# Optimization experiments

Hardware: AMD Instinct MI355X
Metric: run time of the kernel (lower is better)

Reference implementation:

```python
import jax, jax.numpy as jnp
import numpy as np

V, D, H, L, T_MAX = 95, 384, 6, 6, 256
HD = D // H  # 64
FF = 4 * D


def _layernorm(x, scale, bias, eps=1e-5):
    m = jnp.mean(x, axis=-1, keepdims=True)
    v = jnp.var(x, axis=-1, keepdims=True)
    return (x - m) * jax.lax.rsqrt(v + eps) * scale + bias


def setup_inputs() -> dict:
    key = jax.random.key(0)
    ks = iter(jax.random.split(key, 32))
    std = 0.02
    p = {
        "idx": jax.random.randint(next(ks), (128, 256), 0, V, dtype=jnp.int64)
               if jax.config.jax_enable_x64 else
               jax.random.randint(next(ks), (128, 256), 0, V, dtype=jnp.int32),
        "tok_emb": jax.random.normal(next(ks), (V, D), jnp.float32) * std,
        "pos_emb": jax.random.normal(next(ks), (T_MAX, D), jnp.float32) * std,
        # per-layer stacked params [L, ...]
        "ln1_s": jnp.ones((L, D), jnp.float32),
        "ln1_b": jnp.zeros((L, D), jnp.float32),
        "wq": jax.random.normal(next(ks), (L, D, D), jnp.float32) * std,
        "wk": jax.random.normal(next(ks), (L, D, D), jnp.float32) * std,
        "wv": jax.random.normal(next(ks), (L, D, D), jnp.float32) * std,
        "wo": jax.random.normal(next(ks), (L, D, D), jnp.float32) * std,
        "bo": jnp.zeros((L, D), jnp.float32),
        "ln2_s": jnp.ones((L, D), jnp.float32),
        "ln2_b": jnp.zeros((L, D), jnp.float32),
        "w1": jax.random.normal(next(ks), (L, D, FF), jnp.float32) * std,
        "b1": jnp.zeros((L, FF), jnp.float32),
        "w2": jax.random.normal(next(ks), (L, FF, D), jnp.float32) * std,
        "b2": jnp.zeros((L, D), jnp.float32),
        "lnf_s": jnp.ones((D,), jnp.float32),
        "lnf_b": jnp.zeros((D,), jnp.float32),
        "head_w": jax.random.normal(next(ks), (D, V), jnp.float32) * std,
        "head_b": jnp.zeros((V,), jnp.float32),
    }
    return p


def reference(idx, tok_emb, pos_emb, ln1_s, ln1_b, wq, wk, wv, wo, bo,
              ln2_s, ln2_b, w1, b1, w2, b2, lnf_s, lnf_b, head_w, head_b):
    B, T = idx.shape
    x = tok_emb[idx] + pos_emb[:T]  # [B,T,D]
    mask = jnp.tril(jnp.ones((T, T), bool))  # causal
    scale = HD ** -0.5

    def block(x, p):
        s1, b1n, Wq, Wk, Wv, Wo, Bo, s2, b2n, W1, B1, W2, B2 = p
        h = _layernorm(x, s1, b1n)
        q = (h @ Wq).reshape(B, T, H, HD)
        k = (h @ Wk).reshape(B, T, H, HD)
        v = (h @ Wv).reshape(B, T, H, HD)
        scores = jnp.einsum('bqhd,bkhd->bhqk', q, k) * scale
        scores = jnp.where(mask, scores, -jnp.inf)
        wei = jax.nn.softmax(scores, axis=-1)
        attn = jnp.einsum('bhqk,bkhd->bqhd', wei, v).reshape(B, T, D)
        x = x + attn @ Wo + Bo
        h2 = _layernorm(x, s2, b2n)
        x = x + jax.nn.relu(h2 @ W1 + B1) @ W2 + B2
        return x, None

    x, _ = jax.lax.scan(block, x, (ln1_s, ln1_b, wq, wk, wv, wo, bo,
                                   ln2_s, ln2_b, w1, b1, w2, b2))
    logits = _layernorm(x, lnf_s, lnf_b) @ head_w + head_b  # [B,T,V]
    return logits
```

## Files before the change

### kernel.cpp

```cpp
#include <hip/hip_runtime.h>
#include <hip/hip_bf16.h>
#include <cstdint>

#define DEV __device__ __forceinline__

typedef __hip_bfloat16 bf16;
typedef unsigned short u16;
typedef unsigned int u32;
typedef __attribute__((ext_vector_type(8))) short s8v;
typedef __attribute__((ext_vector_type(4))) float f4;

static constexpr int Bn = 128;
static constexpr int Tn = 256;
static constexpr int Dn = 384;
static constexpr int Hn = 6;
static constexpr int HDn = 64;
static constexpr int FFn = 1536;
static constexpr int Vn = 95;
static constexpr int Mn = Bn * 256;

DEV u16 f2b(float f) {
  bf16 h = __float2bfloat16(f);
  return *reinterpret_cast<u16*>(&h);
}
DEV u32 pk2(float a, float b) { return (u32)f2b(a) | ((u32)f2b(b) << 16); }

DEV void gl_lds16(const void* g, void* l) {
  auto gp = (const __attribute__((address_space(1))) u32*)(uintptr_t)g;
  auto lp = (__attribute__((address_space(3))) u32*)(u32)(uintptr_t)l;
  __builtin_amdgcn_global_load_lds(gp, lp, 16, 0, 0);
}

DEV void waitvm(int n) {
  if (n == 0)       asm volatile("s_waitcnt vmcnt(0)" ::: "memory");
  else if (n == 2)  asm volatile("s_waitcnt vmcnt(2)" ::: "memory");
  else if (n == 4)  asm volatile("s_waitcnt vmcnt(4)" ::: "memory");
  else if (n == 6)  asm volatile("s_waitcnt vmcnt(6)" ::: "memory");
  else if (n == 8)  asm volatile("s_waitcnt vmcnt(8)" ::: "memory");
  else if (n == 12) asm volatile("s_waitcnt vmcnt(12)" ::: "memory");
  else              asm volatile("s_waitcnt vmcnt(16)" ::: "memory");
}

template <int MODE, bool RELU, int NKT, int NT>
__global__ __launch_bounds__(256, 2) void gemm_h(
    const u16* __restrict__ A, const u16* __restrict__ Bw,
    const float* __restrict__ bias, const float* __restrict__ resid,
    void* __restrict__ outp)
{
  constexpr int K = NKT * 64;
  constexpr int N = NT * 16;
  constexpr int nTiles = NT / 8;
  __shared__ __align__(16) u16 As[3][128 * 64];
  const int tid = threadIdx.x;
  const int lane = tid & 63, wave = tid >> 6;
  const int quad = lane >> 4, l16 = lane & 15;
  const int wy = wave >> 1, wx = wave & 1;
  const int blk = blockIdx.x;
  const int xcd = blk & 7, tt = blk >> 3;
  const int nT = tt % nTiles, mT = xcd + 8 * (tt / nTiles);
  const int mBase = mT * 128, nBase = nT * 128;

  f4 acc[4][4] = {};

  int rS[4], cS[4];
#pragma unroll
  for (int i = 0; i < 4; i++) {
    int s = i * 256 + tid;
    rS[i] = s >> 3;
    cS[i] = ((s & 7) ^ (rS[i] & 7)) * 8;
  }

  const u16* Ab = A + (size_t)mBase * K;
  const u16* Bp = Bw + (size_t)((nBase >> 4) + wx * 4) * 512 + lane * 8;

#define STAGEA(buf, kt)                                                       \
  do {                                                                        \
    _Pragma("unroll")                                                         \
    for (int i = 0; i < 4; i++)                                               \
      gl_lds16(Ab + (size_t)rS[i] * K + (kt) + cS[i],                         \
               &As[buf][(i * 256 + wave * 64) * 8]);                          \
  } while (0)

  s8v bqa[2][4];
  STAGEA(0, 0);
  __builtin_amdgcn_sched_barrier(0);
#pragma unroll
  for (int j = 0; j < 4; j++)
    bqa[0][j] = *(const s8v*)(Bp + (size_t)0 * (NT * 512) + j * 512);
  __builtin_amdgcn_sched_barrier(0);
  STAGEA(1, 64);
  __builtin_amdgcn_sched_barrier(0);

  const int nk = NKT;
#pragma unroll
  for (int ik = 0; ik < nk; ik++) {
    const int cur = ik % 3;
    const int par = ik & 1;
    waitvm((ik + 1 < nk) ? 4 : 0);
    asm volatile("s_barrier" ::: "memory");
    s8v bqb[4];
#pragma unroll
    for (int j = 0; j < 4; j++)
      bqb[j] = *(const s8v*)(Bp + (size_t)(ik * 2 + 1) * (NT * 512) + j * 512);
    __builtin_amdgcn_sched_barrier(0);
    if (ik + 1 < nk) {
#pragma unroll
      for (int j = 0; j < 4; j++)
        bqa[par ^ 1][j] = *(const s8v*)(Bp + (size_t)(ik * 2 + 2) * (NT * 512) + j * 512);
    }
    __builtin_amdgcn_sched_barrier(0);
    if (ik + 2 < nk) STAGEA((ik + 2) % 3, (ik + 2) * 64);
    __builtin_amdgcn_sched_barrier(0);
    {
      s8v af[4];
#pragma unroll
      for (int i = 0; i < 4; i++) {
        int row = wy * 64 + i * 16 + l16;
        int ch = quad ^ (row & 7);
        af[i] = *(const s8v*)&As[cur][row * 64 + ch * 8];
      }
#pragma unroll
      for (int i = 0; i < 4; i++)
#pragma unroll
        for (int j = 0; j < 4; j++)
          acc[i][j] = __builtin_amdgcn_mfma_f32_16x16x32_bf16(af[i], bqa[par][j], acc[i][j], 0, 0, 0);
    }
    waitvm(4 * ((ik + 1 < nk) + (ik + 2 < nk)));
    {
      s8v af[4];
#pragma unroll
      for (int i = 0; i < 4; i++) {
        int row = wy * 64 + i * 16 + l16;
        int ch = (4 + quad) ^ (row & 7);
        af[i] = *(const s8v*)&As[cur][row * 64 + ch * 8];
      }
#pragma unroll
      for (int i = 0; i < 4; i++)
#pragma unroll
        for (int j = 0; j < 4; j++)
          acc[i][j] = __builtin_amdgcn_mfma_f32_16x16x32_bf16(af[i], bqb[j], acc[i][j], 0, 0, 0);
    }
  }
#undef STAGEA

  if (MODE == 0) {
    u16* out = (u16*)outp;
#pragma unroll
    for (int j = 0; j < 4; j++) {
      int n = nBase + wx * 64 + j * 16 + l16;
      float bv = bias ? bias[n] : 0.f;
#pragma unroll
      for (int i = 0; i < 4; i++) {
        int m0 = mBase + wy * 64 + i * 16 + quad * 4;
#pragma unroll
        for (int r = 0; r < 4; r++) {
          float v = acc[i][j][r] + bv;
          if (RELU) v = fmaxf(v, 0.f);
          out[(size_t)(m0 + r) * N + n] = f2b(v);
        }
      }
    }
  } else if (MODE == 3) {
    float* out = (float*)outp;
#pragma unroll
    for (int j = 0; j < 4; j++) {
      int n = nBase + wx * 64 + j * 16 + l16;
      if (n < Vn) {
        float bv = bias[n];
#pragma unroll
        for (int i = 0; i < 4; i++) {
          int m0 = mBase + wy * 64 + i * 16 + quad * 4;
#pragma unroll
          for (int r = 0; r < 4; r++)
            out[(size_t)(m0 + r) * Vn + n] = acc[i][j][r] + bv;
        }
      }
    }
  } else if (MODE == 4) {
    u16* qb = (u16*)outp;
    u16* kb = qb + (size_t)Mn * 384;
    u16* vb = kb + (size_t)Mn * 384;
#pragma unroll
    for (int j = 0; j < 4; j++) {
      int n = nBase + wx * 64 + j * 16 + l16;
      if (n < 768) {
        u16* dst = (n < 384) ? qb : kb;
        int col = (n < 384) ? n : (n - 384);
#pragma unroll
        for (int i = 0; i < 4; i++) {
          int m0 = mBase + wy * 64 + i * 16 + quad * 4;
#pragma unroll
          for (int r = 0; r < 4; r++)
            dst[(size_t)(m0 + r) * 384 + col] = f2b(acc[i][j][r]);
        }
      } else {
        int n7 = n - 768;
        int hh = n7 >> 6, d = n7 & 63;
#pragma unroll
        for (int i = 0; i < 4; i++) {
          int m0 = mBase + wy * 64 + i * 16 + quad * 4;
          int b = m0 >> 8, t0 = m0 & 255;
          uint2 w;
          w.x = pk2(acc[i][j][0], acc[i][j][1]);
          w.y = pk2(acc[i][j][2], acc[i][j][3]);
          *(uint2*)&vb[((b * Hn + hh) * HDn + d) * Tn + t0] = w;
        }
      }
    }
  }
}

template <int NKT>
__global__ __launch_bounds__(512, 2) void gemm_ln(
    const u16* __restrict__ A, const u16* __restrict__ Bw,
    const float* __restrict__ bias, const float* __restrict__ resid,
    float* __restrict__ xout,
    const float* __restrict__ sc, const float* __restrict__ bi,
    u16* __restrict__ hout)
{
  constexpr int K = NKT * 64;
  constexpr int NT = 24;
  __shared__ __align__(16) u16 As[3][128 * 64];
  __shared__ float2 red[4][128];
  const int tid = threadIdx.x;
  const int lane = tid & 63, wave = tid >> 6;
  const int quad = lane >> 4, l16 = lane & 15;
  const int wy = wave >> 2, wx = wave & 3;
  const int blk = blockIdx.x;
  const int mT = (blk & 7) + 8 * (blk >> 3);
  const int mBase = mT * 128;

  f4 acc[4][6] = {};

  int rS[2], cS[2];
#pragma unroll
  for (int i = 0; i < 2; i++) {
    int s = i * 512 + tid;
    rS[i] = s >> 3;
    cS[i] = ((s & 7) ^ (rS[i] & 7)) * 8;
  }

  const u16* Ab = A + (size_t)mBase * K;
  const u16* Bp = Bw + (size_t)(wx * 6) * 512 + lane * 8;

#define STAGEL(buf, kt)                                                       \
  do {                                                                        \
    _Pragma("unroll")                                                         \
    for (int i = 0; i < 2; i++)                                               \
      gl_lds16(Ab + (size_t)rS[i] * K + (kt) + cS[i],                         \
               &As[buf][(i * 512 + wave * 64) * 8]);                          \
  } while (0)

  STAGEL(0, 0);
  __builtin_amdgcn_sched_barrier(0);
  STAGEL(1, 64);
  __builtin_amdgcn_sched_barrier(0);

  const int nk = NKT;
#pragma unroll
  for (int ik = 0; ik < nk; ik++) {
    const int cur = ik % 3;
    waitvm((ik + 1 < nk) ? 2 : 0);
    asm volatile("s_barrier" ::: "memory");
    s8v bq0[6], bq1[6];
#pragma unroll
    for (int j = 0; j < 6; j++)
      bq0[j] = *(const s8v*)(Bp + (size_t)(ik * 2) * (NT * 512) + j * 512);
    __builtin_amdgcn_sched_barrier(0);
#pragma unroll
    for (int j = 0; j < 6; j++)
      bq1[j] = *(const s8v*)(Bp + (size_t)(ik * 2 + 1) * (NT * 512) + j * 512);
    __builtin_amdgcn_sched_barrier(0);
    if (ik + 2 < nk) STAGEL((ik + 2) % 3, (ik + 2) * 64);
    __builtin_amdgcn_sched_barrier(0);
    waitvm(6 + ((ik + 2 < nk) ? 2 : 0));
    {
      s8v af[4];
#pragma unroll
      for (int i = 0; i < 4; i++) {
        int row = wy * 64 + i * 16 + l16;
        int ch = quad ^ (row & 7);
        af[i] = *(const s8v*)&As[cur][row * 64 + ch * 8];
      }
#pragma unroll
      for (int i = 0; i < 4; i++)
#pragma unroll
        for (int j = 0; j < 6; j++)
          acc[i][j] = __builtin_amdgcn_mfma_f32_16x16x32_bf16(af[i], bq0[j], acc[i][j], 0, 0, 0);
    }
    waitvm((ik + 2 < nk) ? 2 : 0);
    {
      s8v af[4];
#pragma unroll
      for (int i = 0; i < 4; i++) {
        int row = wy * 64 + i * 16 + l16;
        int ch = (4 + quad) ^ (row & 7);
        af[i] = *(const s8v*)&As[cur][row * 64 + ch * 8];
      }
#pragma unroll
      for (int i = 0; i < 4; i++)
#pragma unroll
        for (int j = 0; j < 6; j++)
          acc[i][j] = __builtin_amdgcn_mfma_f32_16x16x32_bf16(af[i], bq1[j], acc[i][j], 0, 0, 0);
    }
  }
#undef STAGEL

  f4 psum[4] = {}, psq[4] = {};
#pragma unroll
  for (int j = 0; j < 6; j++) {
    int n = wx * 96 + j * 16 + l16;
    float bv = bias[n];
#pragma unroll
    for (int i = 0; i < 4; i++) {
      int m0 = mBase + wy * 64 + i * 16 + quad * 4;
#pragma unroll
      for (int r = 0; r < 4; r++) {
        int m = m0 + r;
        float v = resid[(size_t)m * Dn + n] + acc[i][j][r] + bv;
        xout[(size_t)m * Dn + n] = v;
        acc[i][j][r] = v;
        psum[i][r] += v;
        psq[i][r] += v * v;
      }
    }
  }
#pragma unroll
  for (int o = 1; o < 16; o <<= 1)
#pragma unroll
    for (int i = 0; i < 4; i++)
#pragma unroll
      for (int r = 0; r < 4; r++) {
        psum[i][r] += __shfl_xor(psum[i][r], o);
        psq[i][r] += __shfl_xor(psq[i][r], o);
      }
  if (l16 == 0) {
#pragma unroll
    for (int i = 0; i < 4; i++)
#pragma unroll
      for (int r = 0; r < 4; r++) {
        int lr = wy * 64 + i * 16 + quad * 4 + r;
        float2 p; p.x = psum[i][r]; p.y = psq[i][r];
        red[wx][lr] = p;
      }
  }
  __syncthreads();
  float scv[6], biv[6];
#pragma unroll
  for (int j = 0; j < 6; j++) {
    int n = wx * 96 + j * 16 + l16;
    scv[j] = sc[n];
    biv[j] = bi[n];
  }
#pragma unroll
  for (int i = 0; i < 4; i++)
#pragma unroll
    for (int r = 0; r < 4; r++) {
      int lr = wy * 64 + i * 16 + quad * 4 + r;
      float ts = 0.f, tq = 0.f;
#pragma unroll
      for (int w = 0; w < 4; w++) { float2 p = red[w][lr]; ts += p.x; tq += p.y; }
      float mean = ts * (1.f / 384.f);
      float inv = rsqrtf(tq * (1.f / 384.f) - mean * mean + 1e-5f);
      int m = mBase + lr;
#pragma unroll
      for (int j = 0; j < 6; j++) {
        int n = wx * 96 + j * 16 + l16;
        hout[(size_t)m * Dn + n] = f2b((acc[i][j][r] - mean) * inv * scv[j] + biv[j]);
      }
    }
}

__global__ __launch_bounds__(256) void attn_kernel(
    const u16* __restrict__ q, const u16* __restrict__ k,
    const u16* __restrict__ vT, u16* __restrict__ ao)
{
  __shared__ __align__(16) u16 Ps[4][2][16 * 40];
  const int tid = threadIdx.x, lane = tid & 63, wave = tid >> 6;
  const int quad = lane >> 4, l16 = lane & 15;
  const int c4 = blockIdx.x / 768;
  const int bh = blockIdx.x - c4 * 768;
  const int b = bh / Hn, h = bh % Hn;
  const u16* qg = q + (b * Tn) * Dn + h * HDn;
  const u16* kg = k + (b * Tn) * Dn + h * HDn;
  const u16* vg = vT + bh * (HDn * Tn);
  u16* aog = ao + (b * Tn) * Dn + h * HDn;
  const float c1 = 0.125f * 1.44269504f;

  const int qt = (wave & 2) ? ((wave & 1) ? 15 - c4 : 8 + c4)
                            : ((wave & 1) ? 7 - c4 : c4);
  const int qglob = qt * 16 + l16;

  const s8v qf0 = *(const s8v*)&qg[qglob * Dn + quad * 8];
  const s8v qf1 = *(const s8v*)&qg[qglob * Dn + 32 + quad * 8];

  float lsum = 0.f;
  f4 O[4] = {};

  const int nch = qt / 2 + 1;
  for (int c2 = 0; c2 < nch; c2++) {
    const int kk0 = c2 * 32;
    f4 S0 = {0.f, 0.f, 0.f, 0.f}, S1 = S0;
    {
      s8v kf = *(const s8v*)&kg[(kk0 + l16) * Dn + quad * 8];
      S0 = __builtin_amdgcn_mfma_f32_16x16x32_bf16(kf, qf0, S0, 0, 0, 0);
      kf = *(const s8v*)&kg[(kk0 + l16) * Dn + 32 + quad * 8];
      S0 = __builtin_amdgcn_mfma_f32_16x16x32_bf16(kf, qf1, S0, 0, 0, 0);
    }
    if (kk0 + 16 <= qt * 16) {
      s8v kf = *(const s8v*)&kg[(kk0 + 16 + l16) * Dn + quad * 8];
      S1 = __builtin_amdgcn_mfma_f32_16x16x32_bf16(kf, qf0, S1, 0, 0, 0);
      kf = *(const s8v*)&kg[(kk0 + 16 + l16) * Dn + 32 + quad * 8];
      S1 = __builtin_amdgcn_mfma_f32_16x16x32_bf16(kf, qf1, S1, 0, 0, 0);
    }
    const int kkq = kk0 + quad * 4;
    f4 E0, E1;
#pragma unroll
    for (int r = 0; r < 4; r++) {
      E0[r] = (kkq + r <= qglob) ? exp2f(S0[r] * c1) : 0.f;
      E1[r] = (kkq + 16 + r <= qglob) ? exp2f(S1[r] * c1) : 0.f;
      lsum += E0[r] + E1[r];
    }
    u16* prow = &Ps[wave][c2 & 1][l16 * 40];
    uint2 w0, w1;
    w0.x = pk2(E0[0], E0[1]); w0.y = pk2(E0[2], E0[3]);
    w1.x = pk2(E1[0], E1[1]); w1.y = pk2(E1[2], E1[3]);
    *(uint2*)&prow[quad * 4] = w0;
    *(uint2*)&prow[16 + quad * 4] = w1;
    const s8v pf = *(const s8v*)&prow[quad * 8];
#pragma unroll
    for (int dm = 0; dm < 4; dm++) {
      s8v vf = *(const s8v*)&vg[(dm * 16 + l16) * Tn + kk0 + quad * 8];
      O[dm] = __builtin_amdgcn_mfma_f32_16x16x32_bf16(vf, pf, O[dm], 0, 0, 0);
    }
  }

  lsum += __shfl_xor(lsum, 16);
  lsum += __shfl_xor(lsum, 32);
  const float inv = 1.0f / lsum;
#pragma unroll
  for (int dm = 0; dm < 4; dm++) {
    uint2 w;
    w.x = pk2(O[dm][0] * inv, O[dm][1] * inv);
    w.y = pk2(O[dm][2] * inv, O[dm][3] * inv);
    *(uint2*)&aog[qglob * Dn + dm * 16 + quad * 4] = w;
  }
}

__global__ __launch_bounds__(256) void ln_kernel(
    const float* __restrict__ x, const float* __restrict__ sc,
    const float* __restrict__ bi, u16* __restrict__ out)
{
  int tok = blockIdx.x * 4 + (threadIdx.x >> 6);
  int lane = threadIdx.x & 63;
  const float* xr = x + (size_t)tok * Dn;
  float v[6];
  float s = 0.f, sq = 0.f;
#pragma unroll
  for (int i = 0; i < 6; i++) {
    v[i] = xr[lane + 64 * i];
    s += v[i];
    sq += v[i] * v[i];
  }
#pragma unroll
  for (int o = 1; o < 64; o <<= 1) {
    s += __shfl_xor(s, o);
    sq += __shfl_xor(sq, o);
  }
  float mean = s * (1.f / 384.f);
  float var = sq * (1.f / 384.f) - mean * mean;
  float inv = rsqrtf(var + 1e-5f);
  u16* orow = out + (size_t)tok * Dn;
#pragma unroll
  for (int i = 0; i < 6; i++) {
    int c = lane + 64 * i;
    orow[c] = f2b((v[i] - mean) * inv * sc[c] + bi[c]);
  }
}

__global__ __launch_bounds__(256) void embed_kernel(
    const int* __restrict__ idx, const float* __restrict__ tok,
    const float* __restrict__ pos, float* __restrict__ x)
{
  int i = blockIdx.x * 256 + threadIdx.x;
  int m = i / 96, c = (i - m * 96) * 4;
  int t = m & (Tn - 1);
  const float4 tv = *(const float4*)&tok[idx[m] * Dn + c];
  const float4 pv = *(const float4*)&pos[t * Dn + c];
  float4 r;
  r.x = tv.x + pv.x; r.y = tv.y + pv.y; r.z = tv.z + pv.z; r.w = tv.w + pv.w;
  *(float4*)&x[m * Dn + c] = r;
}

__global__ __launch_bounds__(256) void tcvt_frag(
    const float* __restrict__ src, u16* __restrict__ dst,
    int K, int C, int NTsub, int NTtot, int ntoff, int total)
{
  int t = blockIdx.x * 256 + threadIdx.x;
  if (t >= total) return;
  int j8 = t & 7;
  int lane = (t >> 3) & 63;
  int rest = t >> 9;
  int nt = rest % NTsub;
  int lkc = rest / NTsub;
  int KC = K >> 5;
  int kc = lkc % KC;
  int l = lkc / KC;
  int quad = lane >> 4, l16 = lane & 15;
  int k = kc * 32 + quad * 8 + j8;
  int n = nt * 16 + l16;
  float v = (n < C) ? src[((size_t)l * K + k) * C + n] : 0.f;
  dst[((size_t)(l * KC + kc) * NTtot + ntoff + nt) * 512 + lane * 8 + j8] = f2b(v);
}

extern "C" void kernel_launch(void* const* d_in, const int* in_sizes, int n_in,
                              void* d_out, int out_size, void* d_ws, size_t ws_size,
                              hipStream_t stream)
{
  (void)in_sizes; (void)n_in; (void)out_size;
  const int*   idx     = (const int*)d_in[0];
  const float* tok_emb = (const float*)d_in[1];
  const float* pos_emb = (const float*)d_in[2];
  const float* ln1_s   = (const float*)d_in[3];
  const float* ln1_b   = (const float*)d_in[4];
  const float* wq      = (const float*)d_in[5];
  const float* wk      = (const float*)d_in[6];
  const float* wv      = (const float*)d_in[7];
  const float* wo      = (const float*)d_in[8];
  const float* bo      = (const float*)d_in[9];
  const float* ln2_s   = (const float*)d_in[10];
  const float* ln2_b   = (const float*)d_in[11];
  const float* w1      = (const float*)d_in[12];
  const float* b1      = (const float*)d_in[13];
  const float* w2      = (const float*)d_in[14];
  const float* b2      = (const float*)d_in[15];
  const float* lnf_s   = (const float*)d_in[16];
  const float* lnf_b   = (const float*)d_in[17];
  const float* head_w  = (const float*)d_in[18];
  const float* head_b  = (const float*)d_in[19];
  float* out = (float*)d_out;

  char* ws = (char*)d_ws;
  float* x  = (float*)(ws + 0);
  u16*   h  = (u16*)(ws + 50331648);
  u16*   qb = (u16*)(ws + 75497472);
  u16*   kb = (u16*)(ws + 100663296);
  u16*   vb = (u16*)(ws + 125829120);
  u16*   ab = (u16*)(ws + 150994944);
  u16*   f1 = qb;
  u16* qkvT = (u16*)(ws + 176160768);
  u16* woT  = qkvT + 6 * 442368;
  u16* w1T  = woT + 6 * 147456;
  u16* w2T  = w1T + 6 * 589824;
  u16* hdT  = w2T + 6 * 589824;
  if (ws_size < (size_t)197492736) return;

  int tot = 6 * 384 * 384;
  tcvt_frag<<<(tot + 255) / 256, 256, 0, stream>>>(wq, qkvT, 384, 384, 24, 72, 0, tot);
  tcvt_frag<<<(tot + 255) / 256, 256, 0, stream>>>(wk, qkvT, 384, 384, 24, 72, 24, tot);
  tcvt_frag<<<(tot + 255) / 256, 256, 0, stream>>>(wv, qkvT, 384, 384, 24, 72, 48, tot);
  tcvt_frag<<<(tot + 255) / 256, 256, 0, stream>>>(wo, woT, 384, 384, 24, 24, 0, tot);
  tot = 6 * 384 * 1536;
  tcvt_frag<<<(tot + 255) / 256, 256, 0, stream>>>(w1, w1T, 384, 1536, 96, 96, 0, tot);
  tcvt_frag<<<(tot + 255) / 256, 256, 0, stream>>>(w2, w2T, 1536, 384, 24, 24, 0, tot);
  tot = 384 * 128;
  tcvt_frag<<<(tot + 255) / 256, 256, 0, stream>>>(head_w, hdT, 384, 95, 8, 8, 0, tot);

  embed_kernel<<<(Mn * 96) / 256, 256, 0, stream>>>(idx, tok_emb, pos_emb, x);
  ln_kernel<<<Mn / 4, 256, 0, stream>>>(x, ln1_s, ln1_b, h);

  for (int l = 0; l < 6; l++) {
    gemm_h<4, false, 6, 72><<<2304, 256, 0, stream>>>(h, qkvT + l * 442368, nullptr, nullptr, qb);
    attn_kernel<<<Bn * Hn * 4, 256, 0, stream>>>(qb, kb, vb, ab);
    gemm_ln<6><<<256, 512, 0, stream>>>(ab, woT + l * 147456, bo + l * Dn, x, x,
                                        ln2_s + l * Dn, ln2_b + l * Dn, h);
    gemm_h<0, true, 6, 96><<<3072, 256, 0, stream>>>(h, w1T + l * 589824, b1 + l * FFn, nullptr, f1);
    const float* ns = (l < 5) ? (ln1_s + (l + 1) * Dn) : lnf_s;
    const float* nb = (l < 5) ? (ln1_b + (l + 1) * Dn) : lnf_b;
    gemm_ln<24><<<256, 512, 0, stream>>>(f1, w2T + l * 589824, b2 + l * Dn, x, x,
                                         ns, nb, h);
  }
  gemm_h<3, false, 6, 8><<<256, 256, 0, stream>>>(h, hdT, head_b, nullptr, out);
}
```

Baseline: 1.609 ms.

## Stage weight tiles through LDS with double buffering in GEMM kernels

Both GEMM kernels now copy the B (weight) fragments into shared memory with global_load_lds, double-buffered alongside A, instead of each wave loading them directly into registers. The A pipeline drops from triple to double buffering and each iteration waits on vmcnt(0) before the barrier. The goal is to share weight loads across waves that need the same tile and to free registers. In exchange it uses more LDS, which can cap occupancy, and the full wait at the top of every step reduces how much the loads overlap with compute. An unused STAGEBL macro is left behind.

```diff
diff --git a/kernel.cpp b/kernel.cpp
--- a/kernel.cpp
+++ b/kernel.cpp
@@ -31,16 +31,6 @@
   __builtin_amdgcn_global_load_lds(gp, lp, 16, 0, 0);
 }
 
-DEV void waitvm(int n) {
-  if (n == 0)       asm volatile("s_waitcnt vmcnt(0)" ::: "memory");
-  else if (n == 2)  asm volatile("s_waitcnt vmcnt(2)" ::: "memory");
-  else if (n == 4)  asm volatile("s_waitcnt vmcnt(4)" ::: "memory");
-  else if (n == 6)  asm volatile("s_waitcnt vmcnt(6)" ::: "memory");
-  else if (n == 8)  asm volatile("s_waitcnt vmcnt(8)" ::: "memory");
-  else if (n == 12) asm volatile("s_waitcnt vmcnt(12)" ::: "memory");
-  else              asm volatile("s_waitcnt vmcnt(16)" ::: "memory");
-}
-
 template <int MODE, bool RELU, int NKT, int NT>
 __global__ __launch_bounds__(256, 2) void gemm_h(
     const u16* __restrict__ A, const u16* __restrict__ Bw,
@@ -50,7 +40,8 @@
   constexpr int K = NKT * 64;
   constexpr int N = NT * 16;
   constexpr int nTiles = NT / 8;
-  __shared__ __align__(16) u16 As[3][128 * 64];
+  __shared__ __align__(16) u16 As[2][128 * 64];
+  __shared__ __align__(16) u16 Bs[2][8192];
   const int tid = threadIdx.x;
   const int lane = tid & 63, wave = tid >> 6;
   const int quad = lane >> 4, l16 = lane & 15;
@@ -71,7 +62,7 @@
   }
 
   const u16* Ab = A + (size_t)mBase * K;
-  const u16* Bp = Bw + (size_t)((nBase >> 4) + wx * 4) * 512 + lane * 8;
+  const u16* Bp0 = Bw + (size_t)(nBase >> 4) * 512;
 
 #define STAGEA(buf, kt)                                                       \
   do {                                                                        \
@@ -81,67 +72,51 @@
                &As[buf][(i * 256 + wave * 64) * 8]);                          \
   } while (0)
 
-  s8v bqa[2][4];
+#define STAGEB(buf, ikk)                                                      \
+  do {                                                                        \
+    _Pragma("unroll")                                                         \
+    for (int L = 0; L < 4; L++) {                                             \
+      int ks = L >> 1, hf = L & 1;                                            \
+      gl_lds16(Bp0 + (size_t)((ikk) * 2 + ks) * (NT * 512) + hf * 2048 + tid * 8, \
+               &Bs[buf][ks * 4096 + hf * 2048 + tid * 8]);                    \
+    }                                                                         \
+  } while (0)
+
   STAGEA(0, 0);
-  __builtin_amdgcn_sched_barrier(0);
-#pragma unroll
-  for (int j = 0; j < 4; j++)
-    bqa[0][j] = *(const s8v*)(Bp + (size_t)0 * (NT * 512) + j * 512);
-  __builtin_amdgcn_sched_barrier(0);
-  STAGEA(1, 64);
-  __builtin_amdgcn_sched_barrier(0);
+  STAGEB(0, 0);
 
   const int nk = NKT;
 #pragma unroll
   for (int ik = 0; ik < nk; ik++) {
-    const int cur = ik % 3;
-    const int par = ik & 1;
-    waitvm((ik + 1 < nk) ? 4 : 0);
+    const int cur = ik & 1;
+    asm volatile("s_waitcnt vmcnt(0)" ::: "memory");
     asm volatile("s_barrier" ::: "memory");
-    s8v bqb[4];
-#pragma unroll
-    for (int j = 0; j < 4; j++)
-      bqb[j] = *(const s8v*)(Bp + (size_t)(ik * 2 + 1) * (NT * 512) + j * 512);
+    if (ik + 1 < nk) {
+      STAGEA(cur ^ 1, (ik + 1) * 64);
+      STAGEB(cur ^ 1, ik + 1);
+    }
     __builtin_amdgcn_sched_barrier(0);
-    if (ik + 1 < nk) {
-#pragma unroll
-      for (int j = 0; j < 4; j++)
-        bqa[par ^ 1][j] = *(const s8v*)(Bp + (size_t)(ik * 2 + 2) * (NT * 512) + j * 512);
-    }
-    __builtin_amdgcn_sched_barrier(0);
-    if (ik + 2 < nk) STAGEA((ik + 2) % 3, (ik + 2) * 64);
-    __builtin_amdgcn_sched_barrier(0);
-    {
-      s8v af[4];
+#pragma unroll
+    for (int ks = 0; ks < 2; ks++) {
+      s8v af[4], bq[4];
 #pragma unroll
       for (int i = 0; i < 4; i++) {
         int row = wy * 64 + i * 16 + l16;
-        int ch = quad ^ (row & 7);
+        int ch = (ks * 4 + quad) ^ (row & 7);
         af[i] = *(const s8v*)&As[cur][row * 64 + ch * 8];
       }
 #pragma unroll
+      for (int j = 0; j < 4; j++)
+        bq[j] = *(const s8v*)&Bs[cur][ks * 4096 + (wx * 4 + j) * 512 + lane * 8];
+#pragma unroll
       for (int i = 0; i < 4; i++)
 #pragma unroll
         for (int j = 0; j < 4; j++)
-          acc[i][j] = __builtin_amdgcn_mfma_f32_16x16x32_bf16(af[i], bqa[par][j], acc[i][j], 0, 0, 0);
-    }
-    waitvm(4 * ((ik + 1 < nk) + (ik + 2 < nk)));
-    {
-      s8v af[4];
-#pragma unroll
-      for (int i = 0; i < 4; i++) {
-        int row = wy * 64 + i * 16 + l16;
-        int ch = (4 + quad) ^ (row & 7);
-        af[i] = *(const s8v*)&As[cur][row * 64 + ch * 8];
-      }
-#pragma unroll
-      for (int i = 0; i < 4; i++)
-#pragma unroll
-        for (int j = 0; j < 4; j++)
-          acc[i][j] = __builtin_amdgcn_mfma_f32_16x16x32_bf16(af[i], bqb[j], acc[i][j], 0, 0, 0);
+          acc[i][j] = __builtin_amdgcn_mfma_f32_16x16x32_bf16(af[i], bq[j], acc[i][j], 0, 0, 0);
     }
   }
 #undef STAGEA
+#undef STAGEB
 
   if (MODE == 0) {
     u16* out = (u16*)outp;
@@ -220,7 +195,8 @@
 {
   constexpr int K = NKT * 64;
   constexpr int NT = 24;
-  __shared__ __align__(16) u16 As[3][128 * 64];
+  __shared__ __align__(16) u16 As[2][128 * 64];
+  __shared__ __align__(16) u16 Bs[2][24576];
   __shared__ float2 red[4][128];
   const int tid = threadIdx.x;
   const int lane = tid & 63, wave = tid >> 6;
@@ -241,7 +217,6 @@
   }
 
   const u16* Ab = A + (size_t)mBase * K;
-  const u16* Bp = Bw + (size_t)(wx * 6) * 512 + lane * 8;
 
 #define STAGEL(buf, kt)                                                       \
   do {                                                                        \
@@ -251,60 +226,61 @@
                &As[buf][(i * 512 + wave * 64) * 8]);                          \
   } while (0)
 
+#define STAGEBL(buf, ikk)                                                     \
+  do {                                                                        \
+    _Pragma("unroll")                                                         \
+    for (int L = 0; L < 6; L++) {                                             \
+      int ks = L >> 1, th = L & 1;              \
+      (void)ks; (void)th;                                                     \
+    }                                                                         \
+  } while (0)
+
+#define STAGEB2(buf, ikk)                                                     \
+  do {                                                                        \
+    _Pragma("unroll")                                                         \
+    for (int L = 0; L < 6; L++) {                                             \
+      int ks = L / 3, th = L % 3;                                             \
+      int c = th * 4096 + tid * 8;                                            \
+      gl_lds16(Bw + (size_t)((ikk) * 2 + ks) * (NT * 512) + c,                \
+               &Bs[buf][ks * 12288 + c]);                                     \
+    }                                                                         \
+  } while (0)
+
   STAGEL(0, 0);
-  __builtin_amdgcn_sched_barrier(0);
-  STAGEL(1, 64);
-  __builtin_amdgcn_sched_barrier(0);
+  STAGEB2(0, 0);
 
   const int nk = NKT;
 #pragma unroll
   for (int ik = 0; ik < nk; ik++) {
-    const int cur = ik % 3;
-    waitvm((ik + 1 < nk) ? 2 : 0);
+    const int cur = ik & 1;
+    asm volatile("s_waitcnt vmcnt(0)" ::: "memory");
     asm volatile("s_barrier" ::: "memory");
-    s8v bq0[6], bq1[6];
-#pragma unroll
-    for (int j = 0; j < 6; j++)
-      bq0[j] = *(const s8v*)(Bp + (size_t)(ik * 2) * (NT * 512) + j * 512);
+    if (ik + 1 < nk) {
+      STAGEL(cur ^ 1, (ik + 1) * 64);
+      STAGEB2(cur ^ 1, ik + 1);
+    }
     __builtin_amdgcn_sched_barrier(0);
 #pragma unroll
-    for (int j = 0; j < 6; j++)
-      bq1[j] = *(const s8v*)(Bp + (size_t)(ik * 2 + 1) * (NT * 512) + j * 512);
-    __builtin_amdgcn_sched_barrier(0);
-    if (ik + 2 < nk) STAGEL((ik + 2) % 3, (ik + 2) * 64);
-    __builtin_amdgcn_sched_barrier(0);
-    waitvm(6 + ((ik + 2 < nk) ? 2 : 0));
-    {
-      s8v af[4];
+    for (int ks = 0; ks < 2; ks++) {
+      s8v af[4], bq[6];
 #pragma unroll
       for (int i = 0; i < 4; i++) {
         int row = wy * 64 + i * 16 + l16;
-        int ch = quad ^ (row & 7);
+        int ch = (ks * 4 + quad) ^ (row & 7);
         af[i] = *(const s8v*)&As[cur][row * 64 + ch * 8];
       }
 #pragma unroll
+      for (int j = 0; j < 6; j++)
+        bq[j] = *(const s8v*)&Bs[cur][ks * 12288 + (wx * 6 + j) * 512 + lane * 8];
+#pragma unroll
       for (int i = 0; i < 4; i++)
 #pragma unroll
         for (int j = 0; j < 6; j++)
-          acc[i][j] = __builtin_amdgcn_mfma_f32_16x16x32_bf16(af[i], bq0[j], acc[i][j], 0, 0, 0);
-    }
-    waitvm((ik + 2 < nk) ? 2 : 0);
-    {
-      s8v af[4];
-#pragma unroll
-      for (int i = 0; i < 4; i++) {
-        int row = wy * 64 + i * 16 + l16;
-        int ch = (4 + quad) ^ (row & 7);
-        af[i] = *(const s8v*)&As[cur][row * 64 + ch * 8];
-      }
-#pragma unroll
-      for (int i = 0; i < 4; i++)
-#pragma unroll
-        for (int j = 0; j < 6; j++)
-          acc[i][j] = __builtin_amdgcn_mfma_f32_16x16x32_bf16(af[i], bq1[j], acc[i][j], 0, 0, 0);
+          acc[i][j] = __builtin_amdgcn_mfma_f32_16x16x32_bf16(af[i], bq[j], acc[i][j], 0, 0, 0);
     }
   }
 #undef STAGEL
+#undef STAGEB2
 
   f4 psum[4] = {}, psq[4] = {};
 #pragma unroll
```

New measurement: 1.643 ms. 1.02x slower.

## Fuse FFN up/down projections into one kernel and stage gemm_ln weights in LDS

Applied to the files above, without the earlier changes.

Adds an ffn_ln kernel that keeps each 128-row LayerNorm tile in LDS. It loops over 128-wide chunks of the hidden dimension, computing relu(h@W1+b1) into LDS and immediately accumulating it into the W2 product, then applies the residual add and the next LayerNorm. This removes the global write and read of the 1536-wide FFN intermediate and one kernel launch per layer. Separately, gemm_ln now double-buffers both A and the B weight fragments through LDS instead of loading B directly into registers. Both kernels now use large LDS footprints (about 128KB or more), which limits them to one block per CU and serializes the chunk loop behind barriers.

```diff
diff --git a/kernel.cpp b/kernel.cpp
--- a/kernel.cpp
+++ b/kernel.cpp
@@ -220,7 +220,8 @@
 {
   constexpr int K = NKT * 64;
   constexpr int NT = 24;
-  __shared__ __align__(16) u16 As[3][128 * 64];
+  __shared__ __align__(16) u16 As[2][128 * 64];
+  __shared__ __align__(16) u16 Bs[2][24576];
   __shared__ float2 red[4][128];
   const int tid = threadIdx.x;
   const int lane = tid & 63, wave = tid >> 6;
@@ -241,7 +242,6 @@
   }
 
   const u16* Ab = A + (size_t)mBase * K;
-  const u16* Bp = Bw + (size_t)(wx * 6) * 512 + lane * 8;
 
 #define STAGEL(buf, kt)                                                       \
   do {                                                                        \
@@ -251,60 +251,52 @@
                &As[buf][(i * 512 + wave * 64) * 8]);                          \
   } while (0)
 
+#define STAGEB2(buf, ikk)                                                     \
+  do {                                                                        \
+    _Pragma("unroll")                                                         \
+    for (int L = 0; L < 6; L++) {                                             \
+      int ks = L / 3, th = L % 3;                                             \
+      int c = th * 4096 + tid * 8;                                            \
+      gl_lds16(Bw + (size_t)((ikk) * 2 + ks) * (NT * 512) + c,                \
+               &Bs[buf][ks * 12288 + c]);                                     \
+    }                                                                         \
+  } while (0)
+
   STAGEL(0, 0);
-  __builtin_amdgcn_sched_barrier(0);
-  STAGEL(1, 64);
-  __builtin_amdgcn_sched_barrier(0);
+  STAGEB2(0, 0);
 
   const int nk = NKT;
 #pragma unroll
   for (int ik = 0; ik < nk; ik++) {
-    const int cur = ik % 3;
-    waitvm((ik + 1 < nk) ? 2 : 0);
+    const int cur = ik & 1;
+    asm volatile("s_waitcnt vmcnt(0)" ::: "memory");
     asm volatile("s_barrier" ::: "memory");
-    s8v bq0[6], bq1[6];
-#pragma unroll
-    for (int j = 0; j < 6; j++)
-      bq0[j] = *(const s8v*)(Bp + (size_t)(ik * 2) * (NT * 512) + j * 512);
+    if (ik + 1 < nk) {
+      STAGEL(cur ^ 1, (ik + 1) * 64);
+      STAGEB2(cur ^ 1, ik + 1);
+    }
     __builtin_amdgcn_sched_barrier(0);
 #pragma unroll
-    for (int j = 0; j < 6; j++)
-      bq1[j] = *(const s8v*)(Bp + (size_t)(ik * 2 + 1) * (NT * 512) + j * 512);
-    __builtin_amdgcn_sched_barrier(0);
-    if (ik + 2 < nk) STAGEL((ik + 2) % 3, (ik + 2) * 64);
-    __builtin_amdgcn_sched_barrier(0);
-    waitvm(6 + ((ik + 2 < nk) ? 2 : 0));
-    {
-      s8v af[4];
+    for (int ks = 0; ks < 2; ks++) {
+      s8v af[4], bq[6];
 #pragma unroll
       for (int i = 0; i < 4; i++) {
         int row = wy * 64 + i * 16 + l16;
-        int ch = quad ^ (row & 7);
+        int ch = (ks * 4 + quad) ^ (row & 7);
         af[i] = *(const s8v*)&As[cur][row * 64 + ch * 8];
       }
 #pragma unroll
+      for (int j = 0; j < 6; j++)
+        bq[j] = *(const s8v*)&Bs[cur][ks * 12288 + (wx * 6 + j) * 512 + lane * 8];
+#pragma unroll
       for (int i = 0; i < 4; i++)
 #pragma unroll
         for (int j = 0; j < 6; j++)
-          acc[i][j] = __builtin_amdgcn_mfma_f32_16x16x32_bf16(af[i], bq0[j], acc[i][j], 0, 0, 0);
-    }
-    waitvm((ik + 2 < nk) ? 2 : 0);
-    {
-      s8v af[4];
-#pragma unroll
-      for (int i = 0; i < 4; i++) {
-        int row = wy * 64 + i * 16 + l16;
-        int ch = (4 + quad) ^ (row & 7);
-        af[i] = *(const s8v*)&As[cur][row * 64 + ch * 8];
-      }
-#pragma unroll
-      for (int i = 0; i < 4; i++)
-#pragma unroll
-        for (int j = 0; j < 6; j++)
-          acc[i][j] = __builtin_amdgcn_mfma_f32_16x16x32_bf16(af[i], bq1[j], acc[i][j], 0, 0, 0);
+          acc[i][j] = __builtin_amdgcn_mfma_f32_16x16x32_bf16(af[i], bq[j], acc[i][j], 0, 0, 0);
     }
   }
 #undef STAGEL
+#undef STAGEB2
 
   f4 psum[4] = {}, psq[4] = {};
 #pragma unroll
@@ -371,11 +363,205 @@
     }
 }
 
+__global__ __launch_bounds__(512, 2) void ffn_ln(
+    const u16* __restrict__ A, const u16* __restrict__ B1w,
+    const float* __restrict__ b1, const u16* __restrict__ B2w,
+    const float* __restrict__ b2, const float* __restrict__ resid,
+    float* __restrict__ xout,
+    const float* __restrict__ sc, const float* __restrict__ bi,
+    u16* __restrict__ hout)
+{
+  __shared__ __align__(16) u16 Hs[128 * 384];
+  __shared__ __align__(16) u16 Ps[128 * 128];
+  __shared__ float2 red[4][128];
+  const int tid = threadIdx.x;
+  const int lane = tid & 63, wave = tid >> 6;
+  const int quad = lane >> 4, l16 = lane & 15;
+  const int wy = wave >> 2, wx = wave & 3;
+  const int mT = (blockIdx.x & 7) + 8 * (blockIdx.x >> 3);
+  const int mBase = mT * 128;
+  char* Psb = (char*)Ps;
+
+  {
+    const u16* hg = A + (size_t)mBase * Dn;
+#pragma unroll
+    for (int i = 0; i < 12; i++) {
+      u32 S = i * 512 + tid;
+      u32 row = S / 48u;
+      u32 c = S - row * 48u;
+      u32 srcc = (c & ~7u) | ((c & 7u) ^ (row & 7u));
+      gl_lds16(hg + (size_t)row * Dn + srcc * 8, &Hs[S * 8]);
+    }
+  }
+  asm volatile("s_waitcnt vmcnt(0)" ::: "memory");
+  asm volatile("s_barrier" ::: "memory");
+
+  f4 acc2[4][6] = {};
+  const u16* B1p = B1w + (size_t)(wx * 2) * 512 + lane * 8;
+  const u16* B2p = B2w + (size_t)(wx * 6) * 512 + lane * 8;
+  s8v bq2[2][6];
+
+#pragma unroll 1
+  for (int c = 0; c < 12; c++) {
+    float4 b1v0 = *(const float4*)&b1[c * 128 + wx * 32 + quad * 4];
+    float4 b1v1 = *(const float4*)&b1[c * 128 + wx * 32 + 16 + quad * 4];
+    __builtin_amdgcn_sched_barrier(0);
+    s8v bq1[2][4];
+#pragma unroll
+    for (int u = 0; u < 4; u++) {
+      int ks = u >> 1, j = u & 1;
+      bq1[0][u] = *(const s8v*)(B1p + (size_t)(ks * 96 + c * 8 + j) * 512);
+    }
+    __builtin_amdgcn_sched_barrier(0);
+    f4 acc1[4][2] = {};
+#pragma unroll
+    for (int ik = 0; ik < 6; ik++) {
+      const int par = ik & 1;
+      if (ik + 1 < 6) {
+#pragma unroll
+        for (int u = 0; u < 4; u++) {
+          int ks = u >> 1, j = u & 1;
+          bq1[par ^ 1][u] = *(const s8v*)(B1p + (size_t)(((ik + 1) * 2 + ks) * 96 + c * 8 + j) * 512);
+        }
+      }
+      __builtin_amdgcn_sched_barrier(0);
+      waitvm((ik + 1 < 6) ? 4 : 0);
+#pragma unroll
+      for (int ks = 0; ks < 2; ks++) {
+        s8v af[4];
+#pragma unroll
+        for (int i = 0; i < 4; i++) {
+          int row = wy * 64 + i * 16 + l16;
+          int ch = ik * 8 + ((ks * 4 + quad) ^ (row & 7));
+          af[i] = *(const s8v*)&Hs[row * 384 + ch * 8];
+        }
+#pragma unroll
+        for (int i = 0; i < 4; i++)
+#pragma unroll
+          for (int j = 0; j < 2; j++)
+            acc1[i][j] = __builtin_amdgcn_mfma_f32_16x16x32_bf16(
+                bq1[par][ks * 2 + j], af[i], acc1[i][j], 0, 0, 0);
+      }
+    }
+#pragma unroll
+    for (int j = 0; j < 6; j++)
+      bq2[0][j] = *(const s8v*)(B2p + (size_t)((c * 4) * 24 + j) * 512);
+    __builtin_amdgcn_sched_barrier(0);
+#pragma unroll
+    for (int i = 0; i < 4; i++) {
+      int m = wy * 64 + i * 16 + l16;
+#pragma unroll
+      for (int j = 0; j < 2; j++) {
+        float4 bv4 = (j == 0) ? b1v0 : b1v1;
+        float v0 = fmaxf(acc1[i][j][0] + bv4.x, 0.f);
+        float v1 = fmaxf(acc1[i][j][1] + bv4.y, 0.f);
+        float v2 = fmaxf(acc1[i][j][2] + bv4.z, 0.f);
+        float v3 = fmaxf(acc1[i][j][3] + bv4.w, 0.f);
+        uint2 w; w.x = pk2(v0, v1); w.y = pk2(v2, v3);
+        int byteoff = (m * 256 + (wx * 32 + j * 16 + quad * 4) * 2) ^ ((m & 7) << 4);
+        *(uint2*)(Psb + byteoff) = w;
+      }
+    }
+    asm volatile("s_waitcnt lgkmcnt(0)" ::: "memory");
+    asm volatile("s_barrier" ::: "memory");
+#pragma unroll
+    for (int ks2 = 0; ks2 < 4; ks2++) {
+      const int p2 = ks2 & 1;
+      if (ks2 + 1 < 4) {
+#pragma unroll
+        for (int j = 0; j < 6; j++)
+          bq2[p2 ^ 1][j] = *(const s8v*)(B2p + (size_t)((c * 4 + ks2 + 1) * 24 + j) * 512);
+      }
+      __builtin_amdgcn_sched_barrier(0);
+      waitvm((ks2 + 1 < 4) ? 6 : 0);
+      s8v af2[4];
+#pragma unroll
+      for (int i = 0; i < 4; i++) {
+        int m = wy * 64 + i * 16 + l16;
+        int byteoff = (m * 256 + (ks2 * 4 + quad) * 16) ^ ((m & 7) << 4);
+        af2[i] = *(const s8v*)(Psb + byteoff);
+      }
+#pragma unroll
+      for (int i = 0; i < 4; i++)
+#pragma unroll
+        for (int j = 0; j < 6; j++)
+          acc2[i][j] = __builtin_amdgcn_mfma_f32_16x16x32_bf16(
+              af2[i], bq2[p2][j], acc2[i][j], 0, 0, 0);
+    }
+    asm volatile("s_waitcnt lgkmcnt(0)" ::: "memory");
+    asm volatile("s_barrier" ::: "memory");
+  }
+
+  f4 psum[4] = {}, psq[4] = {};
+#pragma unroll
+  for (int j = 0; j < 6; j++) {
+    int n = wx * 96 + j * 16 + l16;
+    float bv = b2[n];
+#pragma unroll
+    for (int i = 0; i < 4; i++) {
+      int m0 = mBase + wy * 64 + i * 16 + quad * 4;
+#pragma unroll
+      for (int r = 0; r < 4; r++) {
+        int m = m0 + r;
+        float v = resid[(size_t)m * Dn + n] + acc2[i][j][r] + bv;
+        xout[(size_t)m * Dn + n] = v;
+        acc2[i][j][r] = v;
+        psum[i][r] += v;
+        psq[i][r] += v * v;
+      }
+    }
+  }
+#pragma unroll
+  for (int o = 1; o < 16; o <<= 1)
+#pragma unroll
+    for (int i = 0; i < 4; i++)
+#pragma unroll
+      for (int r = 0; r < 4; r++) {
+        psum[i][r] += __shfl_xor(psum[i][r], o);
+        psq[i][r] += __shfl_xor(psq[i][r], o);
+      }
+  if (l16 == 0) {
+#pragma unroll
+    for (int i = 0; i < 4; i++)
+#pragma unroll
+      for (int r = 0; r < 4; r++) {
+        int lr = wy * 64 + i * 16 + quad * 4 + r;
+        float2 p; p.x = psum[i][r]; p.y = psq[i][r];
+        red[wx][lr] = p;
+      }
+  }
+  __syncthreads();
+  float scv[6], biv[6];
+#pragma unroll
+  for (int j = 0; j < 6; j++) {
+    int n = wx * 96 + j * 16 + l16;
+    scv[j] = sc[n];
+    biv[j] = bi[n];
+  }
+#pragma unroll
+  for (int i = 0; i < 4; i++)
+#pragma unroll
+    for (int r = 0; r < 4; r++) {
+      int lr = wy * 64 + i * 16 + quad * 4 + r;
+      float ts = 0.f, tq = 0.f;
+#pragma unroll
+      for (int w = 0; w < 4; w++) { float2 p = red[w][lr]; ts += p.x; tq += p.y; }
+      float mean = ts * (1.f / 384.f);
+      float inv = rsqrtf(tq * (1.f / 384.f) - mean * mean + 1e-5f);
+      int m = mBase + lr;
+#pragma unroll
+      for (int j = 0; j < 6; j++) {
+        int n = wx * 96 + j * 16 + l16;
+        hout[(size_t)m * Dn + n] = f2b((acc2[i][j][r] - mean) * inv * scv[j] + biv[j]);
+      }
+    }
+}
+
 __global__ __launch_bounds__(256) void attn_kernel(
     const u16* __restrict__ q, const u16* __restrict__ k,
     const u16* __restrict__ vT, u16* __restrict__ ao)
 {
-  __shared__ __align__(16) u16 Ps[4][2][16 * 40];
+  __shared__ __align__(16) u16 Psh[4][2][16 * 40];
   const int tid = threadIdx.x, lane = tid & 63, wave = tid >> 6;
   const int quad = lane >> 4, l16 = lane & 15;
   const int c4 = blockIdx.x / 768;
@@ -421,7 +607,7 @@
       E1[r] = (kkq + 16 + r <= qglob) ? exp2f(S1[r] * c1) : 0.f;
       lsum += E0[r] + E1[r];
     }
-    u16* prow = &Ps[wave][c2 & 1][l16 * 40];
+    u16* prow = &Psh[wave][c2 & 1][l16 * 40];
     uint2 w0, w1;
     w0.x = pk2(E0[0], E0[1]); w0.y = pk2(E0[2], E0[3]);
     w1.x = pk2(E1[0], E1[1]); w1.y = pk2(E1[2], E1[3]);
@@ -547,7 +733,6 @@
   u16*   kb = (u16*)(ws + 100663296);
   u16*   vb = (u16*)(ws + 125829120);
   u16*   ab = (u16*)(ws + 150994944);
-  u16*   f1 = qb;
   u16* qkvT = (u16*)(ws + 176160768);
   u16* woT  = qkvT + 6 * 442368;
   u16* w1T  = woT + 6 * 147456;
@@ -574,11 +759,11 @@
     attn_kernel<<<Bn * Hn * 4, 256, 0, stream>>>(qb, kb, vb, ab);
     gemm_ln<6><<<256, 512, 0, stream>>>(ab, woT + l * 147456, bo + l * Dn, x, x,
                                         ln2_s + l * Dn, ln2_b + l * Dn, h);
-    gemm_h<0, true, 6, 96><<<3072, 256, 0, stream>>>(h, w1T + l * 589824, b1 + l * FFn, nullptr, f1);
     const float* ns = (l < 5) ? (ln1_s + (l + 1) * Dn) : lnf_s;
     const float* nb = (l < 5) ? (ln1_b + (l + 1) * Dn) : lnf_b;
-    gemm_ln<24><<<256, 512, 0, stream>>>(f1, w2T + l * 589824, b2 + l * Dn, x, x,
-                                         ns, nb, h);
+    ffn_ln<<<256, 512, 0, stream>>>(h, w1T + l * 589824, b1 + l * FFn,
+                                    w2T + l * 589824, b2 + l * Dn,
+                                    x, x, ns, nb, h);
   }
   gemm_h<3, false, 6, 8><<<256, 256, 0, stream>>>(h, hdT, head_b, nullptr, out);
 }
```

Result: faster. 1.458 ms (-9.4%).
